# Optimization experiments

Measured on AMD Instinct MI355X. Metric: run time of the kernel, lower is better.

Reference implementation:

```python
import jax, jax.numpy as jnp
import numpy as np

N_USER = 100_000
N_WALLET = 100_000
E = 1_600_000
HID, OUT = 128, 64
H, C = 4, 32  # GAT heads, per-head channels (HID // 4)
U_IN, W_IN = 16, 4
EPS = 1e-5


def _sage(x_src, x_dst, ei, w_l, b_l, w_r):
    """PyG SAGEConv (mean aggr): lin_l(mean_j x_j) + lin_r(x_i)."""
    src, dst = ei[0], ei[1]
    n = x_dst.shape[0]
    s = jax.ops.segment_sum(x_src[src], dst, num_segments=n)
    deg = jax.ops.segment_sum(jnp.ones((src.shape[0],), x_src.dtype), dst, num_segments=n)
    agg = s / jnp.maximum(deg, 1.0)[:, None]
    return agg @ w_l + b_l + x_dst @ w_r


def _bn(x, g, b):
    """BatchNorm over node dim (training-mode batch stats)."""
    m = x.mean(0)
    v = x.var(0)
    return (x - m) * jax.lax.rsqrt(v + EPS) * g + b


def _segment_softmax(logits, seg, n):
    m = jax.ops.segment_max(logits, seg, num_segments=n)
    e = jnp.exp(logits - m[seg])
    s = jax.ops.segment_sum(e, seg, num_segments=n)
    return e / (s[seg] + 1e-16)


def _gat(x, ei, w, a_src, a_dst, bias):
    """PyG GATConv with self-loops, heads concatenated. Dropout off (eval)."""
    n = x.shape[0]
    loop = jnp.arange(n, dtype=ei.dtype)
    src = jnp.concatenate([ei[0], loop])
    dst = jnp.concatenate([ei[1], loop])
    xp = (x @ w).reshape(n, H, C)                      # [n,H,C]
    al_s = (xp * a_src).sum(-1)                        # [n,H]
    al_d = (xp * a_dst).sum(-1)                        # [n,H]
    logits = jax.nn.leaky_relu(al_s[src] + al_d[dst], 0.2)  # [E+n,H]
    alpha = _segment_softmax(logits, dst, n)
    out = jax.ops.segment_sum(xp[src] * alpha[:, :, None], dst, num_segments=n)
    return out.reshape(n, H * C) + bias


def setup_inputs() -> dict:
    key = jax.random.key(0)
    ks = jax.random.split(key, 24)
    rn = lambda k, s, sc=0.05: jax.random.normal(k, s, jnp.float32) * sc
    ei = lambda k, n: jax.random.randint(k, (2, E), 0, n, jnp.int32)
    return {
        "x_user": rn(ks[0], (N_USER, U_IN), 1.0),
        "x_wallet": rn(ks[1], (N_WALLET, W_IN), 1.0),
        "w_u2w_l": rn(ks[2], (U_IN, HID)), "b_u2w": jnp.zeros((HID,), jnp.float32), "w_u2w_r": rn(ks[3], (W_IN, HID)),
        "w_w2u_l": rn(ks[4], (W_IN, HID)), "b_w2u": jnp.zeros((HID,), jnp.float32), "w_w2u_r": rn(ks[5], (U_IN, HID)),
        "w_u2u_l": rn(ks[6], (U_IN, HID)), "b_u2u": jnp.zeros((HID,), jnp.float32), "w_u2u_r": rn(ks[7], (U_IN, HID)),
        "bn_u_g": jnp.ones((HID,), jnp.float32), "bn_u_b": jnp.zeros((HID,), jnp.float32),
        "bn_w_g": jnp.ones((HID,), jnp.float32), "bn_w_b": jnp.zeros((HID,), jnp.float32),
        "gat_w": rn(ks[8], (HID, H * C)), "gat_as": rn(ks[9], (H, C)), "gat_ad": rn(ks[10], (H, C)),
        "gat_b": jnp.zeros((HID,), jnp.float32),
        "bn2_g": jnp.ones((HID,), jnp.float32), "bn2_b": jnp.zeros((HID,), jnp.float32),
        "proj_w": rn(ks[11], (HID, OUT)), "proj_b": jnp.zeros((OUT,), jnp.float32),
        "ei_uw": ei(ks[12], N_USER),   # src user -> dst wallet (both 100k)
        "ei_wu": ei(ks[13], N_WALLET),  # src wallet -> dst user
        "ei_uu": ei(ks[14], N_USER),
    }


def reference(x_user, x_wallet, w_u2w_l, b_u2w, w_u2w_r, w_w2u_l, b_w2u, w_w2u_r,
              w_u2u_l, b_u2u, w_u2u_r, bn_u_g, bn_u_b, bn_w_g, bn_w_b,
              gat_w, gat_as, gat_ad, gat_b, bn2_g, bn2_b, proj_w, proj_b,
              ei_uw, ei_wu, ei_uu):
    h_w_from_u = jax.nn.relu(_sage(x_user, x_wallet, ei_uw, w_u2w_l, b_u2w, w_u2w_r))
    h_u_from_w = jax.nn.relu(_sage(x_wallet, x_user, ei_wu, w_w2u_l, b_w2u, w_w2u_r))
    h_u_from_u = jax.nn.relu(_sage(x_user, x_user, ei_uu, w_u2u_l, b_u2u, w_u2u_r))
    h_user = _bn(h_u_from_w + h_u_from_u, bn_u_g, bn_u_b)
    _ = _bn(h_w_from_u, bn_w_g, bn_w_b)  # h_wallet: computed in torch module but unused in output
    h_user = jax.nn.relu(_gat(h_user, ei_uu, gat_w, gat_as, gat_ad, gat_b))
    h_user = _bn(h_user, bn2_g, bn2_b)
    return jax.nn.relu(h_user @ proj_w + proj_b)  # dropout = identity (eval)
```

## Files before the change

### kernel.cpp

```cpp
#include <hip/hip_runtime.h>
#include <hip/hip_bf16.h>
#include <cstdint>
#include <cstddef>

#define NN   100000
#define NE   1600000
#define CAP  48

#define NBKT 784
#define BSH  7
#define FB   12
#define BCAP 2432
#define ACHUNK 4096
#define NABLK 391

#define NTILES 1563
#define CH_BN 50
#define NSHAD 4
#define LOG2E 1.44269504088896f

typedef __attribute__((ext_vector_type(8))) short short8;
typedef __attribute__((ext_vector_type(4))) float floatx4;

__device__ inline short f2bs(float x) {
    __hip_bfloat16 h = __float2bfloat16(x);
    return *reinterpret_cast<short*>(&h);
}
__device__ inline int pack2(float a, float b) {
    return ((int)(unsigned short)f2bs(b) << 16) | (unsigned short)f2bs(a);
}
__device__ inline float bflo(unsigned p) { return __uint_as_float(p << 16); }
__device__ inline float bfhi(unsigned p) { return __uint_as_float(p & 0xFFFF0000u); }

#define OFF_PRE   ((size_t)0)
#define OFF_BKTU  ((size_t)0)
#define OFF_BKTW  ((size_t)1906688)
#define OFF_XP    ((size_t)12800000)
#define OFF_AGGU  ((size_t)12800000)
#define OFF_AGGW  ((size_t)14400000)
#define OFF_COLU  ((size_t)19200000)
#define OFF_S1    ((size_t)24000000)
#define OFF_Q1    ((size_t)24000512)
#define OFF_S2    ((size_t)24001024)
#define OFF_Q2    ((size_t)24001536)
#define OFF_CNTU  ((size_t)25600000)
#define OFF_BCUR  ((size_t)25800000)
#define OFF_ALS   ((size_t)25802112)
#define OFF_ALD   ((size_t)26202112)
#define ZBASE     OFF_BCUR
#define ZFLOATS   ((size_t)1600)
#define ZSTATS    ((size_t)2048)

__global__ void __launch_bounds__(256) bin_edges(
    const int* __restrict__ ei_u, const int* __restrict__ ei_w,
    int* __restrict__ bcur_u, int* __restrict__ bkt_u,
    int* __restrict__ bcur_w, int* __restrict__ bkt_w) {
    const int* ei = blockIdx.y ? ei_w : ei_u;
    int* bcur = blockIdx.y ? bcur_w : bcur_u;
    int* bkt  = blockIdx.y ? bkt_w  : bkt_u;
    __shared__ int lcnt[NBKT];
    __shared__ int lbuf[NBKT * FB];
    for (int i = threadIdx.x; i < NBKT; i += 256) lcnt[i] = 0;
    __syncthreads();
    int base = blockIdx.x * ACHUNK;
    #pragma unroll
    for (int k = 0; k < ACHUNK / 256; k++) {
        int e = base + k * 256 + threadIdx.x;
        if (e < NE) {
            int src = ei[e], dst = ei[NE + e];
            int b = dst >> BSH;
            int pk = ((dst & ((1 << BSH) - 1)) << 17) | src;
            int pos = atomicAdd(&lcnt[b], 1);
            if (pos < FB) lbuf[b * FB + pos] = pk;
            else {
                int g = atomicAdd(&bcur[b], 1);
                if (g < BCAP) bkt[(size_t)b * BCAP + g] = pk;
            }
        }
    }
    __syncthreads();
    int wid = threadIdx.x >> 6, lane = threadIdx.x & 63;
    const int BPW = NBKT / 4;
    int b0w = wid * BPW;
    for (int r = 0; r < BPW; r += 64) {
        int rb = r + lane;
        if (rb < BPW) {
            int b = b0w + rb;
            int c = lcnt[b];
            int nn2 = c < FB ? c : FB;
            if (nn2 > 0) {
                int g0 = atomicAdd(&bcur[b], nn2);
                for (int i2 = 0; i2 < nn2; i2++) {
                    int g = g0 + i2;
                    if (g < BCAP) bkt[(size_t)b * BCAP + g] = lbuf[b * FB + i2];
                }
            }
        }
    }
}

__global__ void __launch_bounds__(256) csr_agg(
    const int* __restrict__ bcur_u, const int* __restrict__ bkt_u,
    int* __restrict__ cnt_g, int* __restrict__ col_g,
    const float* __restrict__ xu, float* __restrict__ aggu,
    const int* __restrict__ bcur_w, const int* __restrict__ bkt_w,
    const float* __restrict__ xw, float* __restrict__ aggw) {
    int type = blockIdx.y;
    const int* bcur = type ? bcur_w : bcur_u;
    const int* bkt  = type ? bkt_w  : bkt_u;
    int B = blockIdx.x;
    int node_base = B << BSH;
    if (node_base >= NN) return;
    __shared__ int cnt[128];
    __shared__ int col[128 * CAP];
    if (threadIdx.x < 128) cnt[threadIdx.x] = 0;
    __syncthreads();
    int n = bcur[B]; if (n > BCAP) n = BCAP;
    const int* bp = bkt + (size_t)B * BCAP;
    for (int i = threadIdx.x; i < n; i += 256) {
        int p = bp[i];
        int d = p >> 17;
        int pos = atomicAdd(&cnt[d], 1);
        if (pos < CAP) col[d * CAP + pos] = p & 0x1FFFF;
    }
    __syncthreads();
    int nn_here = NN - node_base; if (nn_here > 128) nn_here = 128;
    int wv = threadIdx.x >> 6, lane = threadIdx.x & 63;

    if (type == 0) {
        if (threadIdx.x < nn_here) cnt_g[node_base + threadIdx.x] = cnt[threadIdx.x];
        int total4 = nn_here * CAP / 4;
        const int4* cs = (const int4*)col;
        int4* cg = (int4*)(col_g + (size_t)node_base * CAP);
        for (int i = threadIdx.x; i < total4; i += 256) cg[i] = cs[i];
        int j = lane >> 2, kq = lane & 3;
        const float4* xu4 = (const float4*)xu;
        for (int nl = wv * 32; nl < wv * 32 + 32; nl += 2) {
            if (nl >= nn_here) break;
            int degA = cnt[nl];
            int degB = (nl + 1 < nn_here) ? cnt[nl + 1] : 0;
            int nuA = degA < CAP ? degA : CAP;
            int nuB = degB < CAP ? degB : CAP;
            float4 vA = make_float4(0.f, 0.f, 0.f, 0.f);
            float4 vB = make_float4(0.f, 0.f, 0.f, 0.f);
            #pragma unroll
            for (int it = 0; it < 3; it++) {
                int bb = j + (it << 4);
                int sA = (bb < nuA) ? col[nl * CAP + bb] : 0;
                int sB = (bb < nuB) ? col[(nl + 1) * CAP + bb] : 0;
                float4 xA = xu4[(size_t)sA * 4 + kq];
                float4 xB = xu4[(size_t)sB * 4 + kq];
                if (bb < nuA) { vA.x += xA.x; vA.y += xA.y; vA.z += xA.z; vA.w += xA.w; }
                if (bb < nuB) { vB.x += xB.x; vB.y += xB.y; vB.z += xB.z; vB.w += xB.w; }
            }
            #pragma unroll
            for (int m = 4; m <= 32; m <<= 1) {
                vA.x += __shfl_xor(vA.x, m, 64); vA.y += __shfl_xor(vA.y, m, 64);
                vA.z += __shfl_xor(vA.z, m, 64); vA.w += __shfl_xor(vA.w, m, 64);
                vB.x += __shfl_xor(vB.x, m, 64); vB.y += __shfl_xor(vB.y, m, 64);
                vB.z += __shfl_xor(vB.z, m, 64); vB.w += __shfl_xor(vB.w, m, 64);
            }
            if (lane < 4) {
                float rA = 1.f / fmaxf((float)degA, 1.f);
                float4 oA = make_float4(vA.x * rA, vA.y * rA, vA.z * rA, vA.w * rA);
                *(float4*)&aggu[(size_t)(node_base + nl) * 16 + 4 * lane] = oA;
                if (nl + 1 < nn_here) {
                    float rB = 1.f / fmaxf((float)degB, 1.f);
                    float4 oB = make_float4(vB.x * rB, vB.y * rB, vB.z * rB, vB.w * rB);
                    *(float4*)&aggu[(size_t)(node_base + nl + 1) * 16 + 4 * lane] = oB;
                }
            }
        }
    } else {
        const float4* xw4 = (const float4*)xw;
        for (int nl = wv * 32; nl < wv * 32 + 32; nl += 2) {
            if (nl >= nn_here) break;
            int degA = cnt[nl];
            int degB = (nl + 1 < nn_here) ? cnt[nl + 1] : 0;
            int nwA = degA < CAP ? degA : CAP;
            int nwB = degB < CAP ? degB : CAP;
            int sA = (lane < nwA) ? col[nl * CAP + lane] : 0;
            int sB = (lane < nwB) ? col[(nl + 1) * CAP + lane] : 0;
            float4 xA = xw4[sA];
            float4 xB = xw4[sB];
            float4 vA = (lane < nwA) ? xA : make_float4(0.f, 0.f, 0.f, 0.f);
            float4 vB = (lane < nwB) ? xB : make_float4(0.f, 0.f, 0.f, 0.f);
            #pragma unroll
            for (int m = 1; m <= 32; m <<= 1) {
                vA.x += __shfl_xor(vA.x, m, 64); vA.y += __shfl_xor(vA.y, m, 64);
                vA.z += __shfl_xor(vA.z, m, 64); vA.w += __shfl_xor(vA.w, m, 64);
                vB.x += __shfl_xor(vB.x, m, 64); vB.y += __shfl_xor(vB.y, m, 64);
                vB.z += __shfl_xor(vB.z, m, 64); vB.w += __shfl_xor(vB.w, m, 64);
            }
            if (lane == 0) {
                float rA = 1.f / fmaxf((float)degA, 1.f);
                float4 oA = make_float4(vA.x * rA, vA.y * rA, vA.z * rA, vA.w * rA);
                *(float4*)&aggw[(size_t)(node_base + nl) * 4] = oA;
                if (nl + 1 < nn_here) {
                    float rB = 1.f / fmaxf((float)degB, 1.f);
                    float4 oB = make_float4(vB.x * rB, vB.y * rB, vB.z * rB, vB.w * rB);
                    *(float4*)&aggw[(size_t)(node_base + nl + 1) * 4] = oB;
                }
            }
        }
    }
}

__global__ void __launch_bounds__(256, 2) sage_gemm(
    const float* __restrict__ aggu, const float* __restrict__ aggw,
    const float* __restrict__ xu,
    const float* __restrict__ wl_w2u, const float* __restrict__ b_w2u, const float* __restrict__ wr_w2u,
    const float* __restrict__ wl_u2u, const float* __restrict__ b_u2u, const float* __restrict__ wr_u2u,
    __hip_bfloat16* __restrict__ pre,
    float* __restrict__ bnsum, float* __restrict__ bnsq) {
    __shared__ short lw[16 * 64 * 8];
    __shared__ short la[64 * 136];
    __shared__ float lbs[128], lbq[128];
    int tid = threadIdx.x;
    for (int idx = tid; idx < 8192; idx += 256) {
        int mat = idx >> 12;
        int k = (idx >> 7) & 31, n = idx & 127;
        float w;
        if (mat == 0)
            w = (k < 4) ? wl_w2u[k * 128 + n] : (k < 20 ? wr_w2u[(k - 4) * 128 + n] : 0.f);
        else
            w = (k < 16) ? wl_u2u[k * 128 + n] : wr_u2u[(k - 16) * 128 + n];
        int t = n >> 4, l15 = n & 15, q = (k >> 3) & 3, j = k & 7;
        lw[((mat * 8 + t) * 64 + q * 16 + l15) * 8 + j] = f2bs(w);
    }
    if (tid < 128) { lbs[tid] = 0.f; lbq[tid] = 0.f; }
    __syncthreads();
    int wv = tid >> 6, lane = tid & 63;
    int quad = lane >> 4, l15 = lane & 15;
    short8 w1[8], w2[8];
    #pragma unroll
    for (int t = 0; t < 8; t++) {
        w1[t] = *(const short8*)&lw[(t * 64 + lane) * 8];
        w2[t] = *(const short8*)&lw[((8 + t) * 64 + lane) * 8];
    }
    float bw[8], bu[8];
    #pragma unroll
    for (int t = 0; t < 8; t++) {
        bw[t] = b_w2u[t * 16 + l15];
        bu[t] = b_u2u[t * 16 + l15];
    }
    float sE[8], qE[8];
    #pragma unroll
    for (int t = 0; t < 8; t++) { sE[t] = 0.f; qE[t] = 0.f; }
    for (int tile = blockIdx.x; tile < NTILES; tile += gridDim.x) {
        int nbase = tile * 64;
        __syncthreads();
        {
            int node = tid >> 2, p = tid & 3;
            int gn = nbase + node;
            float4 v = make_float4(0.f, 0.f, 0.f, 0.f);
            if (gn < NN) v = *(const float4*)&xu[(size_t)gn * 16 + 4 * p];
            int2 pk; pk.x = pack2(v.x, v.y); pk.y = pack2(v.z, v.w);
            *(int2*)&la[node * 136 + 4 + 4 * p] = pk;
            *(int2*)&la[node * 136 + 48 + 4 * p] = pk;
        }
        {
            int node = tid >> 2, p = tid & 3;
            int gn = nbase + node;
            float4 v = make_float4(0.f, 0.f, 0.f, 0.f);
            if (gn < NN) v = *(const float4*)&aggu[(size_t)gn * 16 + 4 * p];
            int2 pk; pk.x = pack2(v.x, v.y); pk.y = pack2(v.z, v.w);
            *(int2*)&la[node * 136 + 32 + 4 * p] = pk;
        }
        if (tid < 64) {
            int node = tid, gn = nbase + node;
            float4 v = make_float4(0.f, 0.f, 0.f, 0.f);
            if (gn < NN) v = *(const float4*)&aggw[(size_t)gn * 4];
            int2 pk; pk.x = pack2(v.x, v.y); pk.y = pack2(v.z, v.w);
            *(int2*)&la[node * 136 + 0] = pk;
            int2 z; z.x = 0; z.y = 0;
            *(int2*)&la[node * 136 + 20] = z;
            *(int2*)&la[node * 136 + 24] = z;
            *(int2*)&la[node * 136 + 28] = z;
        }
        __syncthreads();
        short8 af1 = *(const short8*)&la[(wv * 16 + l15) * 136 + quad * 8];
        short8 af2 = *(const short8*)&la[(wv * 16 + l15) * 136 + 32 + quad * 8];
        floatx4 acc1[8], acc2[8];
        #pragma unroll
        for (int t = 0; t < 8; t++) {
            acc1[t] = (floatx4){0.f, 0.f, 0.f, 0.f};
            acc2[t] = (floatx4){0.f, 0.f, 0.f, 0.f};
        }
        #pragma unroll
        for (int t = 0; t < 8; t++) {
            acc1[t] = __builtin_amdgcn_mfma_f32_16x16x32_bf16(af1, w1[t], acc1[t], 0, 0, 0);
            acc2[t] = __builtin_amdgcn_mfma_f32_16x16x32_bf16(af2, w2[t], acc2[t], 0, 0, 0);
        }
        __syncthreads();
        #pragma unroll
        for (int t = 0; t < 8; t++)
            #pragma unroll
            for (int r = 0; r < 4; r++) {
                float v1 = fmaxf(acc1[t][r] + bw[t], 0.f);
                float v2 = fmaxf(acc2[t][r] + bu[t], 0.f);
                short vv = f2bs(v1 + v2);
                la[(wv * 16 + quad * 4 + r) * 136 + t * 16 + l15] = vv;
                int node = nbase + wv * 16 + quad * 4 + r;
                if (node < NN) {
                    float vr = __uint_as_float(((unsigned)(unsigned short)vv) << 16);
                    sE[t] += vr; qE[t] += vr * vr;
                }
            }
        __syncthreads();
        #pragma unroll
        for (int c = 0; c < 4; c++) {
            int idx = c * 256 + tid;
            int node = idx >> 4, f8 = (idx & 15) * 8;
            int gn = nbase + node;
            if (gn < NN)
                *(int4*)(pre + (size_t)gn * 128 + f8) = *(const int4*)&la[node * 136 + f8];
        }
    }
    __syncthreads();
    #pragma unroll
    for (int t = 0; t < 8; t++) {
        atomicAdd(&lbs[t * 16 + l15], sE[t]);
        atomicAdd(&lbq[t * 16 + l15], qE[t]);
    }
    __syncthreads();
    if (tid < 128) {
        int sh = (blockIdx.x & (NSHAD - 1)) << 7;
        atomicAdd(&bnsum[sh + tid], lbs[tid]);
        atomicAdd(&bnsq[sh + tid], lbq[tid]);
    }
}

__global__ void __launch_bounds__(256) bn_stats_act2(const unsigned* __restrict__ x2,
                                                     const float* __restrict__ gb,
                                                     float* __restrict__ sum, float* __restrict__ sq) {
    int f2 = threadIdx.x & 63, half = threadIdx.x >> 6;
    int n0 = blockIdx.x * CH_BN;
    float gb0 = gb[2 * f2], gb1 = gb[2 * f2 + 1];
    float s0 = 0.f, q0 = 0.f, s1 = 0.f, q1 = 0.f;
    for (int i = n0 + half; i < n0 + CH_BN; i += 4) {
        unsigned p = x2[(size_t)i * 64 + f2];
        float v0 = fmaxf(bflo(p) + gb0, 0.f), v1 = fmaxf(bfhi(p) + gb1, 0.f);
        s0 += v0; q0 += v0 * v0; s1 += v1; q1 += v1 * v1;
    }
    __shared__ float a0[256], c0[256], a1[256], c1[256];
    a0[threadIdx.x] = s0; c0[threadIdx.x] = q0;
    a1[threadIdx.x] = s1; c1[threadIdx.x] = q1;
    __syncthreads();
    if (half == 0) {
        for (int h = 1; h < 4; h++) {
            s0 += a0[h * 64 + f2]; q0 += c0[h * 64 + f2];
            s1 += a1[h * 64 + f2]; q1 += c1[h * 64 + f2];
        }
        int sh = (blockIdx.x & (NSHAD - 1)) << 7;
        atomicAdd(&sum[sh + 2 * f2], s0);     atomicAdd(&sq[sh + 2 * f2], q0);
        atomicAdd(&sum[sh + 2 * f2 + 1], s1); atomicAdd(&sq[sh + 2 * f2 + 1], q1);
    }
}

__global__ void __launch_bounds__(256, 2) gemm_al(
    const unsigned* __restrict__ pre2, const float* __restrict__ s1, const float* __restrict__ q1,
    const float* __restrict__ bng, const float* __restrict__ bnb,
    const float* __restrict__ gw, const float* __restrict__ gas, const float* __restrict__ gad,
    __hip_bfloat16* __restrict__ xp, float* __restrict__ al_s, float* __restrict__ al_d) {
    __shared__ short lw[32 * 64 * 8];
    __shared__ short la[64 * 136];
    __shared__ float lsc[128], lsh[128];
    int tid = threadIdx.x;
    if (tid < 128) {
        float sv = s1[tid] + s1[128 + tid] + s1[256 + tid] + s1[384 + tid];
        float qv = q1[tid] + q1[128 + tid] + q1[256 + tid] + q1[384 + tid];
        float m = sv * (1.0f / NN);
        float v = qv * (1.0f / NN) - m * m;
        float sc = bng[tid] * rsqrtf(v + 1e-5f);
        lsc[tid] = sc; lsh[tid] = bnb[tid] - m * sc;
    }
    for (int idx = tid; idx < 16384; idx += 256) {
        int k = idx >> 7, n = idx & 127;
        int t = n >> 4, l15 = n & 15, s = k >> 5, q = (k >> 3) & 3, j = k & 7;
        lw[(((t * 4 + s) * 64) + q * 16 + l15) * 8 + j] = f2bs(gw[idx]);
    }
    __syncthreads();
    int wv = tid >> 6, lane = tid & 63;
    int quad = lane >> 4, l15 = lane & 15;
    short8 wfrag[8][4];
    #pragma unroll
    for (int t = 0; t < 8; t++)
        #pragma unroll
        for (int s = 0; s < 4; s++)
            wfrag[t][s] = *(const short8*)&lw[((t * 4 + s) * 64 + lane) * 8];
    float asv[8], adv[8];
    #pragma unroll
    for (int t = 0; t < 8; t++) {
        asv[t] = gas[t * 16 + l15] * LOG2E;
        adv[t] = gad[t * 16 + l15] * LOG2E;
    }
    for (int tile = blockIdx.x; tile < NTILES; tile += gridDim.x) {
        int nbase = tile * 64;
        __syncthreads();
        #pragma unroll
        for (int c = 0; c < 8; c++) {
            int idx = c * 256 + tid;
            int node = idx >> 5, g = idx & 31;
            uint2 pp = make_uint2(0u, 0u);
            int gn = nbase + node;
            if (gn < NN) pp = *(const uint2*)&pre2[(size_t)gn * 64 + 2 * g];
            int f = 4 * g;
            float v0 = bflo(pp.x), v1 = bfhi(pp.x), v2 = bflo(pp.y), v3 = bfhi(pp.y);
            int2 pk;
            pk.x = pack2(v0 * lsc[f] + lsh[f],         v1 * lsc[f + 1] + lsh[f + 1]);
            pk.y = pack2(v2 * lsc[f + 2] + lsh[f + 2], v3 * lsc[f + 3] + lsh[f + 3]);
            *(int2*)&la[node * 136 + f] = pk;
        }
        __syncthreads();
        short8 af[4];
        #pragma unroll
        for (int s = 0; s < 4; s++)
            af[s] = *(const short8*)&la[(wv * 16 + l15) * 136 + s * 32 + quad * 8];
        floatx4 acc[8];
        #pragma unroll
        for (int t = 0; t < 8; t++) acc[t] = (floatx4){0.f, 0.f, 0.f, 0.f};
        #pragma unroll
        for (int s = 0; s < 4; s++)
            #pragma unroll
            for (int t = 0; t < 8; t++)
                acc[t] = __builtin_amdgcn_mfma_f32_16x16x32_bf16(af[s], wfrag[t][s], acc[t], 0, 0, 0);
        #pragma unroll
        for (int r = 0; r < 4; r++) {
            int node = nbase + wv * 16 + quad * 4 + r;
            #pragma unroll
            for (int h = 0; h < 4; h++) {
                float vs = acc[2 * h][r] * asv[2 * h] + acc[2 * h + 1][r] * asv[2 * h + 1];
                float vd = acc[2 * h][r] * adv[2 * h] + acc[2 * h + 1][r] * adv[2 * h + 1];
                #pragma unroll
                for (int m = 8; m >= 1; m >>= 1) {
                    vs += __shfl_xor(vs, m, 64);
                    vd += __shfl_xor(vd, m, 64);
                }
                if (l15 == 0 && node < NN) {
                    al_s[(size_t)node * 4 + h] = vs;
                    al_d[(size_t)node * 4 + h] = vd;
                }
            }
        }
        __syncthreads();
        #pragma unroll
        for (int t = 0; t < 8; t++)
            #pragma unroll
            for (int r = 0; r < 4; r++)
                la[(wv * 16 + quad * 4 + r) * 136 + t * 16 + l15] = f2bs(acc[t][r]);
        __syncthreads();
        #pragma unroll
        for (int c = 0; c < 4; c++) {
            int idx = c * 256 + tid;
            int node = idx >> 4, f8 = (idx & 15) * 8;
            int gn = nbase + node;
            if (gn < NN)
                *(int4*)(xp + (size_t)gn * 128 + f8) = *(const int4*)&la[node * 136 + f8];
        }
    }
}

__global__ void __launch_bounds__(256, 2) gemm_proj(
    const unsigned* __restrict__ gat2, const float* __restrict__ gb,
    const float* __restrict__ s2, const float* __restrict__ q2,
    const float* __restrict__ bng, const float* __restrict__ bnb,
    const float* __restrict__ pw, const float* __restrict__ pb,
    float* __restrict__ out) {
    __shared__ short lw[16 * 64 * 8];
    __shared__ short la[64 * 136];
    __shared__ float lsc[128], lsh[128], lgb[128];
    int tid = threadIdx.x;
    if (tid < 128) {
        float sv = s2[tid] + s2[128 + tid] + s2[256 + tid] + s2[384 + tid];
        float qv = q2[tid] + q2[128 + tid] + q2[256 + tid] + q2[384 + tid];
        float m = sv * (1.0f / NN);
        float v = qv * (1.0f / NN) - m * m;
        float sc = bng[tid] * rsqrtf(v + 1e-5f);
        lsc[tid] = sc; lsh[tid] = bnb[tid] - m * sc;
        lgb[tid] = gb[tid];
    }
    for (int idx = tid; idx < 8192; idx += 256) {
        int k = idx >> 6, n = idx & 63;
        int t = n >> 4, l15 = n & 15, s = k >> 5, q = (k >> 3) & 3, j = k & 7;
        lw[(((t * 4 + s) * 64) + q * 16 + l15) * 8 + j] = f2bs(pw[idx]);
    }
    __syncthreads();
    int wv = tid >> 6, lane = tid & 63;
    int quad = lane >> 4, l15 = lane & 15;
    short8 wfrag[4][4];
    #pragma unroll
    for (int t = 0; t < 4; t++)
        #pragma unroll
        for (int s = 0; s < 4; s++)
            wfrag[t][s] = *(const short8*)&lw[((t * 4 + s) * 64 + lane) * 8];
    float pbv[4];
    #pragma unroll
    for (int t = 0; t < 4; t++) pbv[t] = pb[t * 16 + l15];
    for (int tile = blockIdx.x; tile < NTILES; tile += gridDim.x) {
        int nbase = tile * 64;
        __syncthreads();
        #pragma unroll
        for (int c = 0; c < 8; c++) {
            int idx = c * 256 + tid;
            int node = idx >> 5, g = idx & 31;
            uint2 pp = make_uint2(0u, 0u);
            int gn = nbase + node;
            if (gn < NN) pp = *(const uint2*)&gat2[(size_t)gn * 64 + 2 * g];
            int f = 4 * g;
            float h0 = fmaxf(bflo(pp.x) + lgb[f],     0.f) * lsc[f]     + lsh[f];
            float h1 = fmaxf(bfhi(pp.x) + lgb[f + 1], 0.f) * lsc[f + 1] + lsh[f + 1];
            float h2 = fmaxf(bflo(pp.y) + lgb[f + 2], 0.f) * lsc[f + 2] + lsh[f + 2];
            float h3 = fmaxf(bfhi(pp.y) + lgb[f + 3], 0.f) * lsc[f + 3] + lsh[f + 3];
            int2 pk; pk.x = pack2(h0, h1); pk.y = pack2(h2, h3);
            *(int2*)&la[node * 136 + f] = pk;
        }
        __syncthreads();
        short8 af[4];
        #pragma unroll
        for (int s = 0; s < 4; s++)
            af[s] = *(const short8*)&la[(wv * 16 + l15) * 136 + s * 32 + quad * 8];
        floatx4 acc[4];
        #pragma unroll
        for (int t = 0; t < 4; t++) acc[t] = (floatx4){0.f, 0.f, 0.f, 0.f};
        #pragma unroll
        for (int s = 0; s < 4; s++)
            #pragma unroll
            for (int t = 0; t < 4; t++)
                acc[t] = __builtin_amdgcn_mfma_f32_16x16x32_bf16(af[s], wfrag[t][s], acc[t], 0, 0, 0);
        #pragma unroll
        for (int r = 0; r < 4; r++) {
            int gn = nbase + wv * 16 + quad * 4 + r;
            if (gn < NN) {
                #pragma unroll
                for (int t = 0; t < 4; t++)
                    out[(size_t)gn * 64 + t * 16 + l15] = fmaxf(acc[t][r] + pbv[t], 0.f);
            }
        }
    }
}

__global__ void __launch_bounds__(256) gat_gather(
    const int* __restrict__ cnt_u, const int* __restrict__ col_u,
    const float* __restrict__ al_s, const float* __restrict__ al_d,
    const unsigned* __restrict__ xp2, unsigned* __restrict__ gout2) {
    int i = (blockIdx.x * 256 + threadIdx.x) >> 6;
    int lane = threadIdx.x & 63;
    int g = lane >> 4, q = lane & 15;
    int h = q >> 2;
    float ad = al_d[(size_t)i * 4 + h];
    int deg = cnt_u[i];
    int n = deg < CAP ? deg : CAP;
    int mycol = (lane < n) ? col_u[(size_t)i * CAP + lane] : 0;
    float a0 = 0.f, a1 = 0.f, a2 = 0.f, a3 = 0.f;
    float a4 = 0.f, a5 = 0.f, a6 = 0.f, a7 = 0.f, den = 0.f;
    if (g == 0) {
        float l = al_s[(size_t)i * 4 + h] + ad;
        float e = exp2f(fmaxf(l, 0.2f * l));
        uint4 p = *(const uint4*)&xp2[(size_t)i * 64 + 4 * q];
        a0 = e * bflo(p.x); a1 = e * bfhi(p.x);
        a2 = e * bflo(p.y); a3 = e * bfhi(p.y);
        a4 = e * bflo(p.z); a5 = e * bfhi(p.z);
        a6 = e * bflo(p.w); a7 = e * bfhi(p.w);
        den = e;
    }
    for (int b = 0; b < n; b += 16) {
        int s[4]; float A[4]; uint4 p[4];
        #pragma unroll
        for (int u = 0; u < 4; u++)
            s[u] = __shfl(mycol, b + 4 * u + g, 64);
        #pragma unroll
        for (int u = 0; u < 4; u++)
            A[u] = al_s[(size_t)s[u] * 4 + h];
        #pragma unroll
        for (int u = 0; u < 4; u++)
            p[u] = *(const uint4*)&xp2[(size_t)s[u] * 64 + 4 * q];
        #pragma unroll
        for (int u = 0; u < 4; u++) {
            float l = A[u] + ad;
            float e = (b + 4 * u + g < n) ? exp2f(fmaxf(l, 0.2f * l)) : 0.f;
            a0 += e * bflo(p[u].x); a1 += e * bfhi(p[u].x);
            a2 += e * bflo(p[u].y); a3 += e * bfhi(p[u].y);
            a4 += e * bflo(p[u].z); a5 += e * bfhi(p[u].z);
            a6 += e * bflo(p[u].w); a7 += e * bfhi(p[u].w);
            den += e;
        }
    }
    a0 += __shfl_xor(a0, 16, 64); a0 += __shfl_xor(a0, 32, 64);
    a1 += __shfl_xor(a1, 16, 64); a1 += __shfl_xor(a1, 32, 64);
    a2 += __shfl_xor(a2, 16, 64); a2 += __shfl_xor(a2, 32, 64);
    a3 += __shfl_xor(a3, 16, 64); a3 += __shfl_xor(a3, 32, 64);
    a4 += __shfl_xor(a4, 16, 64); a4 += __shfl_xor(a4, 32, 64);
    a5 += __shfl_xor(a5, 16, 64); a5 += __shfl_xor(a5, 32, 64);
    a6 += __shfl_xor(a6, 16, 64); a6 += __shfl_xor(a6, 32, 64);
    a7 += __shfl_xor(a7, 16, 64); a7 += __shfl_xor(a7, 32, 64);
    den += __shfl_xor(den, 16, 64); den += __shfl_xor(den, 32, 64);
    if (g == 0) {
        float r = 1.0f / (den + 1e-16f);
        uint4 o;
        o.x = (unsigned)pack2(a0 * r, a1 * r);
        o.y = (unsigned)pack2(a2 * r, a3 * r);
        o.z = (unsigned)pack2(a4 * r, a5 * r);
        o.w = (unsigned)pack2(a6 * r, a7 * r);
        *(uint4*)&gout2[(size_t)i * 64 + 4 * q] = o;
    }
}

extern "C" void kernel_launch(void* const* d_in, const int* in_sizes, int n_in,
                              void* d_out, int out_size, void* d_ws, size_t ws_size,
                              hipStream_t stream) {
    const float* x_user   = (const float*)d_in[0];
    const float* x_wallet = (const float*)d_in[1];
    const float* w_w2u_l  = (const float*)d_in[5];
    const float* b_w2u    = (const float*)d_in[6];
    const float* w_w2u_r  = (const float*)d_in[7];
    const float* w_u2u_l  = (const float*)d_in[8];
    const float* b_u2u    = (const float*)d_in[9];
    const float* w_u2u_r  = (const float*)d_in[10];
    const float* bn_u_g   = (const float*)d_in[11];
    const float* bn_u_b   = (const float*)d_in[12];
    const float* gat_w    = (const float*)d_in[15];
    const float* gat_as   = (const float*)d_in[16];
    const float* gat_ad   = (const float*)d_in[17];
    const float* gat_b    = (const float*)d_in[18];
    const float* bn2_g    = (const float*)d_in[19];
    const float* bn2_b    = (const float*)d_in[20];
    const float* proj_w   = (const float*)d_in[21];
    const float* proj_b   = (const float*)d_in[22];
    const int* ei_wu      = (const int*)d_in[24];
    const int* ei_uu      = (const int*)d_in[25];
    float* out = (float*)d_out;
    float* ws  = (float*)d_ws;

    unsigned* pre2 = (unsigned*)(ws + OFF_PRE);
    __hip_bfloat16* pre = (__hip_bfloat16*)(ws + OFF_PRE);
    int*   bkt_u  = (int*)(ws + OFF_BKTU);
    int*   bkt_w  = (int*)(ws + OFF_BKTW);
    __hip_bfloat16* xp = (__hip_bfloat16*)(ws + OFF_XP);
    unsigned* xp2 = (unsigned*)(ws + OFF_XP);
    float* aggu = ws + OFF_AGGU;
    float* aggw = ws + OFF_AGGW;
    int*   col_u  = (int*)(ws + OFF_COLU);
    int*   cnt_u  = (int*)(ws + OFF_CNTU);
    int*   bcur_u = (int*)(ws + OFF_BCUR);
    int*   bcur_w = (int*)(ws + OFF_BCUR) + 800;
    float* al_s = ws + OFF_ALS, *al_d = ws + OFF_ALD;
    float* s1 = ws + OFF_S1, *q1 = ws + OFF_Q1;
    float* s2 = ws + OFF_S2, *q2 = ws + OFF_Q2;

    hipMemsetAsync(ws + ZBASE, 0, ZFLOATS * sizeof(float), stream);
    hipMemsetAsync(ws + OFF_S1, 0, ZSTATS * sizeof(float), stream);

    bin_edges<<<dim3(NABLK, 2), 256, 0, stream>>>(ei_uu, ei_wu, bcur_u, bkt_u, bcur_w, bkt_w);

    csr_agg<<<dim3(NBKT, 2), 256, 0, stream>>>(
        bcur_u, bkt_u, cnt_u, col_u, x_user, aggu,
        bcur_w, bkt_w, x_wallet, aggw);

    sage_gemm<<<512, 256, 0, stream>>>(
        aggu, aggw, x_user, w_w2u_l, b_w2u, w_w2u_r, w_u2u_l, b_u2u, w_u2u_r,
        pre, s1, q1);

    gemm_al<<<512, 256, 0, stream>>>(pre2, s1, q1, bn_u_g, bn_u_b,
                                     gat_w, gat_as, gat_ad, xp, al_s, al_d);

    unsigned* gat2 = pre2;
    gat_gather<<<NN / 4, 256, 0, stream>>>(cnt_u, col_u, al_s, al_d, xp2, gat2);

    bn_stats_act2<<<NN / CH_BN, 256, 0, stream>>>(gat2, gat_b, s2, q2);

    gemm_proj<<<512, 256, 0, stream>>>(gat2, gat_b, s2, q2, bn2_g, bn2_b,
                                       proj_w, proj_b, out);
}
```

Before: 421.7 us.

## Retune edge binning, merge workspace memsets, and rework user neighbor aggregation mapping

Doubles the edge chunk per binning block (halving its grid) and enlarges the per-bucket shared staging buffer, relocating the bucket counters next to the stats so a single memset clears both. The user-side mean aggregation now assigns four nodes per wave, with 16 lanes per node, and loops only up to the actual maximum degree among those nodes instead of a fixed three iterations over CAP. This reduces wasted gathers on padded neighbor slots and cuts one memset launch, at the cost of fewer binning blocks and more shared memory per block.

```diff
diff --git a/kernel.cpp b/kernel.cpp
--- a/kernel.cpp
+++ b/kernel.cpp
@@ -9,10 +9,10 @@
 
 #define NBKT 784
 #define BSH  7
-#define FB   12
+#define FB   16
 #define BCAP 2432
-#define ACHUNK 4096
-#define NABLK 391
+#define ACHUNK 8192
+#define NABLK 196
 
 #define NTILES 1563
 #define CH_BN 50
@@ -43,13 +43,12 @@
 #define OFF_Q1    ((size_t)24000512)
 #define OFF_S2    ((size_t)24001024)
 #define OFF_Q2    ((size_t)24001536)
+#define OFF_BCUR  ((size_t)24002048)
 #define OFF_CNTU  ((size_t)25600000)
-#define OFF_BCUR  ((size_t)25800000)
 #define OFF_ALS   ((size_t)25802112)
 #define OFF_ALD   ((size_t)26202112)
-#define ZBASE     OFF_BCUR
-#define ZFLOATS   ((size_t)1600)
-#define ZSTATS    ((size_t)2048)
+#define ZBASE     OFF_S1
+#define ZFLOATS   ((size_t)3648)
 
 __global__ void __launch_bounds__(256) bin_edges(
     const int* __restrict__ ei_u, const int* __restrict__ ei_w,
@@ -63,7 +62,7 @@
     for (int i = threadIdx.x; i < NBKT; i += 256) lcnt[i] = 0;
     __syncthreads();
     int base = blockIdx.x * ACHUNK;
-    #pragma unroll
+    #pragma unroll 4
     for (int k = 0; k < ACHUNK / 256; k++) {
         int e = base + k * 256 + threadIdx.x;
         if (e < NE) {
@@ -133,41 +132,37 @@
         const int4* cs = (const int4*)col;
         int4* cg = (int4*)(col_g + (size_t)node_base * CAP);
         for (int i = threadIdx.x; i < total4; i += 256) cg[i] = cs[i];
-        int j = lane >> 2, kq = lane & 3;
+        int kq = lane & 3, nd = (lane >> 2) & 3, sl = lane >> 4;
         const float4* xu4 = (const float4*)xu;
-        for (int nl = wv * 32; nl < wv * 32 + 32; nl += 2) {
-            if (nl >= nn_here) break;
-            int degA = cnt[nl];
-            int degB = (nl + 1 < nn_here) ? cnt[nl + 1] : 0;
-            int nuA = degA < CAP ? degA : CAP;
-            int nuB = degB < CAP ? degB : CAP;
-            float4 vA = make_float4(0.f, 0.f, 0.f, 0.f);
-            float4 vB = make_float4(0.f, 0.f, 0.f, 0.f);
-            #pragma unroll
-            for (int it = 0; it < 3; it++) {
-                int bb = j + (it << 4);
-                int sA = (bb < nuA) ? col[nl * CAP + bb] : 0;
-                int sB = (bb < nuB) ? col[(nl + 1) * CAP + bb] : 0;
-                float4 xA = xu4[(size_t)sA * 4 + kq];
-                float4 xB = xu4[(size_t)sB * 4 + kq];
-                if (bb < nuA) { vA.x += xA.x; vA.y += xA.y; vA.z += xA.z; vA.w += xA.w; }
-                if (bb < nuB) { vB.x += xB.x; vB.y += xB.y; vB.z += xB.z; vB.w += xB.w; }
-            }
-            #pragma unroll
-            for (int m = 4; m <= 32; m <<= 1) {
-                vA.x += __shfl_xor(vA.x, m, 64); vA.y += __shfl_xor(vA.y, m, 64);
-                vA.z += __shfl_xor(vA.z, m, 64); vA.w += __shfl_xor(vA.w, m, 64);
-                vB.x += __shfl_xor(vB.x, m, 64); vB.y += __shfl_xor(vB.y, m, 64);
-                vB.z += __shfl_xor(vB.z, m, 64); vB.w += __shfl_xor(vB.w, m, 64);
-            }
-            if (lane < 4) {
-                float rA = 1.f / fmaxf((float)degA, 1.f);
-                float4 oA = make_float4(vA.x * rA, vA.y * rA, vA.z * rA, vA.w * rA);
-                *(float4*)&aggu[(size_t)(node_base + nl) * 16 + 4 * lane] = oA;
-                if (nl + 1 < nn_here) {
-                    float rB = 1.f / fmaxf((float)degB, 1.f);
-                    float4 oB = make_float4(vB.x * rB, vB.y * rB, vB.z * rB, vB.w * rB);
-                    *(float4*)&aggu[(size_t)(node_base + nl + 1) * 16 + 4 * lane] = oB;
+        for (int nb = wv * 32; nb < wv * 32 + 32; nb += 4) {
+            int myn = nb + nd;
+            int deg = cnt[myn];
+            int nu = deg < CAP ? deg : CAP;
+            int numax = nu;
+            numax = max(numax, __shfl_xor(numax, 4, 64));
+            numax = max(numax, __shfl_xor(numax, 8, 64));
+            int iters2 = (numax + 7) >> 3;
+            float4 v = make_float4(0.f, 0.f, 0.f, 0.f);
+            for (int it = 0; it < iters2; it++) {
+                int b0 = sl + (it << 3);
+                int b1 = b0 + 4;
+                int s0 = (b0 < nu) ? col[myn * CAP + b0] : 0;
+                int s1 = (b1 < nu) ? col[myn * CAP + b1] : 0;
+                float4 x0 = xu4[(size_t)s0 * 4 + kq];
+                float4 x1 = xu4[(size_t)s1 * 4 + kq];
+                if (b0 < nu) { v.x += x0.x; v.y += x0.y; v.z += x0.z; v.w += x0.w; }
+                if (b1 < nu) { v.x += x1.x; v.y += x1.y; v.z += x1.z; v.w += x1.w; }
+            }
+            v.x += __shfl_xor(v.x, 16, 64); v.y += __shfl_xor(v.y, 16, 64);
+            v.z += __shfl_xor(v.z, 16, 64); v.w += __shfl_xor(v.w, 16, 64);
+            v.x += __shfl_xor(v.x, 32, 64); v.y += __shfl_xor(v.y, 32, 64);
+            v.z += __shfl_xor(v.z, 32, 64); v.w += __shfl_xor(v.w, 32, 64);
+            if (lane < 16) {
+                int wn = nb + (lane >> 2);
+                if (wn < nn_here) {
+                    float r = 1.f / fmaxf((float)cnt[wn], 1.f);
+                    float4 o = make_float4(v.x * r, v.y * r, v.z * r, v.w * r);
+                    *(float4*)&aggu[(size_t)(node_base + wn) * 16 + 4 * (lane & 3)] = o;
                 }
             }
         }
@@ -649,7 +644,6 @@
     float* s2 = ws + OFF_S2, *q2 = ws + OFF_Q2;
 
     hipMemsetAsync(ws + ZBASE, 0, ZFLOATS * sizeof(float), stream);
-    hipMemsetAsync(ws + OFF_S1, 0, ZSTATS * sizeof(float), stream);
 
     bin_edges<<<dim3(NABLK, 2), 256, 0, stream>>>(ei_uu, ei_wu, bcur_u, bkt_u, bcur_w, bkt_w);
 
```

Measured after the change: 408.3 us. 3.2% less time.
